# Performance work log

Hardware: AMD Instinct MI355X
Metric: run time of the kernel (lower is better)

## Reference

```python
import jax, jax.numpy as jnp
import numpy as np

SOS, EOS = 0, 1
MAXLEN = 128
EPS = 1e-5


def setup_inputs() -> dict:
    key = jax.random.key(0)
    ks = jax.random.split(key, 10)
    B, T, Hc, Hs, V, Hm = 64, 1024, 512, 512, 64, 128
    h = jax.random.normal(ks[0], (B, T, Hc), dtype=jnp.float32)
    x_seq_lens = jax.random.randint(ks[1], (B,), 1, T + 1).astype(jnp.int32)
    s = 0.05
    return {
        "h": h,
        "W_ih": jax.random.normal(ks[2], (4 * Hs, V + Hc), dtype=jnp.float32) * s,
        "W_hh": jax.random.normal(ks[3], (4 * Hs, Hs), dtype=jnp.float32) * s,
        "b_ih": jax.random.normal(ks[4], (4 * Hs,), dtype=jnp.float32) * s,
        "b_hh": jax.random.normal(ks[5], (4 * Hs,), dtype=jnp.float32) * s,
        "fc1_w": jax.random.normal(ks[6], (Hm, Hs + Hc), dtype=jnp.float32) * s,
        "fc1_b": jax.random.normal(ks[7], (Hm,), dtype=jnp.float32) * s,
        "fc2_w": jax.random.normal(ks[8], (V, Hm), dtype=jnp.float32) * s,
        "x_seq_lens": x_seq_lens,
    }


def reference(h, W_ih, W_hh, b_ih, b_hh, fc1_w, fc1_b, fc2_w, x_seq_lens):
    B, T, Hc = h.shape
    Hs = W_hh.shape[1]
    V = fc2_w.shape[0]
    # attention length mask [B, T]
    mask = (jnp.arange(T)[None, :] < x_seq_lens[:, None]).astype(h.dtype)
    sos = jax.nn.one_hot(jnp.full((B,), SOS), V, dtype=h.dtype)
    x0 = jnp.concatenate([sos, h[:, 0, :]], axis=-1)  # [B, V+Hc]
    carry0 = (x0, jnp.zeros((B, Hs), h.dtype), jnp.zeros((B, Hs), h.dtype),
              jnp.full((B,), MAXLEN, jnp.int32))

    def step(carry, t):
        x, hs, cs, lens = carry
        # single-layer LSTM cell, torch gate order i,f,g,o
        gates = x @ W_ih.T + hs @ W_hh.T + b_ih + b_hh
        i, f, g, o = jnp.split(gates, 4, axis=-1)
        cs = jax.nn.sigmoid(f) * cs + jax.nn.sigmoid(i) * jnp.tanh(g)
        hs = jax.nn.sigmoid(o) * jnp.tanh(cs)
        # dot-product attention (apply_proj=False, num_heads=1)
        e = jnp.einsum('bd,btd->bt', hs, h)
        exps = jnp.exp(e - jnp.max(e)) * mask  # MaskedSoftmax: global-max shift
        a = exps / (exps.sum(-1, keepdims=True) + EPS)
        ctx = jnp.einsum('bt,btd->bd', a, h)
        # chardist: two stacked linears (no nonlinearity), then softmax
        feat = jnp.concatenate([hs, ctx], axis=-1)
        logits = (feat @ fc1_w.T + fc1_b) @ fc2_w.T
        y_hat = jax.nn.softmax(logits, axis=-1)
        hit = (jnp.argmax(y_hat, axis=-1) == EOS) & (lens > t)
        lens = jnp.where(hit, t + 1, lens)
        x = jnp.concatenate([y_hat, ctx], axis=-1)  # decode mode (y=None)
        return (x, hs, cs, lens), (y_hat, a)

    (_, _, _, lens), (y_hats, atts) = jax.lax.scan(step, carry0, jnp.arange(MAXLEN))
    y_hats = jnp.transpose(y_hats, (1, 0, 2))              # [B, L, V]
    attentions = jnp.transpose(atts, (1, 0, 2))[:, None]   # [B, 1, L, T]
    return y_hats, lens, attentions
```

## Files before the change

kernel.cpp:

```cpp
#include <hip/hip_runtime.h>
#include <math.h>

typedef unsigned short ushort_t;
typedef unsigned int uint_t;

#define OFF_XT    0
#define OFF_CS    102400
#define OFF_E     135168
#define OFF_MD    200704
#define OFF_LENS  202752
#define OFF_W2    202816
#define OFF_B2    268352
#define OFF_CP    268416
#define OFF_HB16F 793600
#define WS_NEED   ((size_t)(793600 + 16777216) * 4)

#define OUT_YH   0
#define OUT_LENS 524288
#define OUT_ATT  524352

__device__ __forceinline__ float sigf(float x) { return 1.0f / (1.0f + __expf(-x)); }
__device__ __forceinline__ float dot4(float4 a, float4 b) {
    return a.x * b.x + a.y * b.y + a.z * b.z + a.w * b.w;
}
__device__ __forceinline__ uint_t bf16rne(float x) {
    uint_t u = __float_as_uint(x);
    return (u + 0x7FFFu + ((u >> 16) & 1u)) >> 16;
}
#define BLO(u) __uint_as_float((u) << 16)
#define BHI(u) __uint_as_float((u) & 0xFFFF0000u)

__global__ void k_init(const float* __restrict__ h, float* __restrict__ ws) {
    int blk = blockIdx.x, tid = threadIdx.x;
    int idx = blk * 256 + tid;
    if (idx < 102400) {
        int k = idx >> 6, b = idx & 63;
        float v = 0.0f;
        if (k == 0) v = 1.0f;
        else if (k >= 64 && k < 576) v = h[(size_t)b * 524288 + (k - 64)];
        ws[OFF_XT + idx] = v;
    }
    if (blk >= 400 && blk < 528)
        ws[OFF_CS + (blk - 400) * 256 + tid] = 0.0f;
    if (blk == 527 && tid < 64) ((int*)ws)[OFF_LENS + tid] = 128;
}

__global__ void k_hconv(const float* __restrict__ h, float* __restrict__ ws) {
    size_t i = ((size_t)blockIdx.x * 256 + threadIdx.x) * 8;
    float4 a = *(const float4*)(h + i);
    float4 b = *(const float4*)(h + i + 4);
    uint4 o;
    o.x = bf16rne(a.x) | (bf16rne(a.y) << 16);
    o.y = bf16rne(a.z) | (bf16rne(a.w) << 16);
    o.z = bf16rne(b.x) | (bf16rne(b.y) << 16);
    o.w = bf16rne(b.z) | (bf16rne(b.w) << 16);
    *(uint4*)((ushort_t*)(ws + OFF_HB16F) + i) = o;
}

__global__ void k_fuse(const float* __restrict__ fc1w, const float* __restrict__ fc1b,
                       const float* __restrict__ fc2w, float* __restrict__ ws) {
    int blk = blockIdx.x;
    int v = blk >> 2, kc = blk & 3;
    int k = kc * 256 + threadIdx.x;
    float acc = 0.0f;
#pragma unroll 8
    for (int m = 0; m < 128; m++) acc += fc2w[v * 128 + m] * fc1w[(size_t)m * 1024 + k];
    ws[OFF_W2 + (size_t)v * 1024 + k] = acc;
    if (kc == 0 && threadIdx.x == 0) {
        float bb = 0.0f;
        for (int m = 0; m < 128; m++) bb += fc2w[v * 128 + m] * fc1b[m];
        ws[OFF_B2 + v] = bb;
    }
}

__global__ void k_gates(const float* __restrict__ Wih, const float* __restrict__ Whh,
                        const float* __restrict__ bih, const float* __restrict__ bhh,
                        float* __restrict__ ws, int p) {
    const int tid = threadIdx.x;
    const int lane = tid & 63;
    const int w = tid >> 6;
    const int hs_in  = 576 + (p ? 512 : 0);
    const int hs_out = 576 + (p ? 0 : 512);
    __shared__ float gpart[4096];
    const int u0 = blockIdx.x * 2;
    const int wq = __builtin_amdgcn_readfirstlane(w);
    float acc[2][4] = {{0, 0, 0, 0}, {0, 0, 0, 0}};
    int k0 = wq * 136, k1 = k0 + 136;
    int kx1 = k1 < 576 ? k1 : 576;
#pragma unroll 2
    for (int k = k0; k < kx1; k += 4) {
        float4 xv;
        xv.x = ws[OFF_XT + (k + 0) * 64 + lane];
        xv.y = ws[OFF_XT + (k + 1) * 64 + lane];
        xv.z = ws[OFF_XT + (k + 2) * 64 + lane];
        xv.w = ws[OFF_XT + (k + 3) * 64 + lane];
#pragma unroll
        for (int uu = 0; uu < 2; ++uu)
#pragma unroll
            for (int g = 0; g < 4; ++g)
                acc[uu][g] += dot4(*(const float4*)&Wih[(size_t)(g * 512 + u0 + uu) * 576 + k], xv);
    }
    int kh0 = k0 > 576 ? k0 : 576;
#pragma unroll 2
    for (int k = kh0; k < k1; k += 4) {
        float4 xv;
        xv.x = ws[OFF_XT + (hs_in + (k - 576) + 0) * 64 + lane];
        xv.y = ws[OFF_XT + (hs_in + (k - 576) + 1) * 64 + lane];
        xv.z = ws[OFF_XT + (hs_in + (k - 576) + 2) * 64 + lane];
        xv.w = ws[OFF_XT + (hs_in + (k - 576) + 3) * 64 + lane];
#pragma unroll
        for (int uu = 0; uu < 2; ++uu)
#pragma unroll
            for (int g = 0; g < 4; ++g)
                acc[uu][g] += dot4(*(const float4*)&Whh[(size_t)(g * 512 + u0 + uu) * 512 + (k - 576)], xv);
    }
#pragma unroll
    for (int uu = 0; uu < 2; ++uu)
#pragma unroll
        for (int g = 0; g < 4; ++g)
            gpart[((w * 2 + uu) * 4 + g) * 64 + lane] = acc[uu][g];
    __syncthreads();
    if (tid < 128) {
        int uu = tid >> 6, b = tid & 63;
        int u = u0 + uu;
        float g4[4];
#pragma unroll
        for (int g = 0; g < 4; ++g) {
            float s = 0.0f;
#pragma unroll
            for (int ww = 0; ww < 8; ++ww) s += gpart[((ww * 2 + uu) * 4 + g) * 64 + b];
            g4[g] = s + bih[g * 512 + u] + bhh[g * 512 + u];
        }
        int idx = u * 64 + b;
        float co = ws[OFF_CS + idx];
        float I = sigf(g4[0]), F = sigf(g4[1]), G = tanhf(g4[2]), O = sigf(g4[3]);
        float cn = F * co + I * G;
        ws[OFF_CS + idx] = cn;
        ws[OFF_XT + (size_t)(hs_out + u) * 64 + b] = O * tanhf(cn);
    }
}

__global__ void k_attn16(const int* __restrict__ slen, float* __restrict__ ws, int p) {
    const int blk = blockIdx.x;
    const int tid = threadIdx.x;
    const int lane = tid & 63;
    const int w = tid >> 6;
    const int hs_out = 576 + (p ? 0 : 512);
    const int b = blk >> 4, sb = blk & 15;
    const int L = slen[b];
    const int t0 = sb * 64;
    __shared__ ushort_t stage[2][8192];
    __shared__ float hs_sh[512];
    __shared__ float e_sh[16];
    const ushort_t* hb = (const ushort_t*)(ws + OFF_HB16F) + ((size_t)b * 1024 + t0) * 512;
    uint4 r0 = *(const uint4*)(hb + tid * 8);
    uint4 r1 = *(const uint4*)(hb + 2048 + tid * 8);
    uint4 r2 = *(const uint4*)(hb + 4096 + tid * 8);
    uint4 r3 = *(const uint4*)(hb + 6144 + tid * 8);
    hs_sh[tid]       = ws[OFF_XT + (size_t)(hs_out + tid) * 64 + b];
    hs_sh[256 + tid] = ws[OFF_XT + (size_t)(hs_out + 256 + tid) * 64 + b];
    __syncthreads();
    float hsv[8];
#pragma unroll
    for (int j = 0; j < 8; ++j) hsv[j] = hs_sh[lane * 8 + j];
    float m_run = -INFINITY, D = 0.0f, accx = 0.0f, accy = 0.0f;
    int buf = 0;
    for (int c = 0; c < 4; ++c) {
        *(uint4*)&stage[buf][tid * 8]        = r0;
        *(uint4*)&stage[buf][tid * 8 + 2048] = r1;
        *(uint4*)&stage[buf][tid * 8 + 4096] = r2;
        *(uint4*)&stage[buf][tid * 8 + 6144] = r3;
        __syncthreads();
        if (c < 3) {
            const ushort_t* g = hb + (size_t)(c + 1) * 8192;
            r0 = *(const uint4*)(g + tid * 8);
            r1 = *(const uint4*)(g + 2048 + tid * 8);
            r2 = *(const uint4*)(g + 4096 + tid * 8);
            r3 = *(const uint4*)(g + 6144 + tid * 8);
        }
#pragma unroll
        for (int rr = 0; rr < 4; ++rr) {
            int tl = w * 4 + rr;
            uint4 hv = *(const uint4*)&stage[buf][tl * 512 + lane * 8];
            float part = BLO(hv.x) * hsv[0] + BHI(hv.x) * hsv[1]
                       + BLO(hv.y) * hsv[2] + BHI(hv.y) * hsv[3]
                       + BLO(hv.z) * hsv[4] + BHI(hv.z) * hsv[5]
                       + BLO(hv.w) * hsv[6] + BHI(hv.w) * hsv[7];
#pragma unroll
            for (int mm = 1; mm < 64; mm <<= 1) part += __shfl_xor(part, mm);
            if (lane == 0) {
                e_sh[tl] = part;
                ws[OFF_E + (size_t)b * 1024 + t0 + c * 16 + tl] = part;
            }
        }
        __syncthreads();
        float cm = e_sh[0];
#pragma unroll
        for (int j = 1; j < 16; ++j) cm = fmaxf(cm, e_sh[j]);
        float m_new = fmaxf(m_run, cm);
        float sc = __expf(m_run - m_new);
        accx *= sc; accy *= sc; D *= sc;
        m_run = m_new;
        const uint_t* st32 = (const uint_t*)&stage[buf][0];
#pragma unroll
        for (int tl = 0; tl < 16; ++tl) {
            int tg = t0 + c * 16 + tl;
            float wt = (tg < L) ? __expf(e_sh[tl] - m_run) : 0.0f;
            D += wt;
            uint_t v = st32[tl * 256 + tid];
            accx += wt * BLO(v);
            accy += wt * BHI(v);
        }
        buf ^= 1;
    }
    float2 o2; o2.x = accx; o2.y = accy;
    *(float2*)&ws[OFF_CP + (size_t)(b * 16 + sb) * 512 + tid * 2] = o2;
    if (tid == 0) {
        ws[OFF_MD + (b * 16 + sb) * 2]     = m_run;
        ws[OFF_MD + (b * 16 + sb) * 2 + 1] = D;
    }
}

__global__ void k_attn(const float* __restrict__ h, const int* __restrict__ slen,
                       float* __restrict__ ws, int p) {
    const int blk = blockIdx.x;
    const int tid = threadIdx.x;
    const int lane = tid & 63;
    const int w = tid >> 6;
    const int hs_out = 576 + (p ? 0 : 512);
    const int b = blk >> 4, sb = blk & 15;
    const int L = slen[b];
    const int t0 = sb * 64;
    __shared__ float stage[4096];
    __shared__ float hs_sh[512];
    __shared__ float e_sh[8];
    const float* hb = h + ((size_t)b * 1024 + t0) * 512;
    hs_sh[tid]       = ws[OFF_XT + (size_t)(hs_out + tid) * 64 + b];
    hs_sh[256 + tid] = ws[OFF_XT + (size_t)(hs_out + 256 + tid) * 64 + b];
    __syncthreads();
    float hsv[8];
#pragma unroll
    for (int j = 0; j < 8; ++j) hsv[j] = hs_sh[lane * 8 + j];
    float m_run = -INFINITY, D = 0.0f, accx = 0.0f, accy = 0.0f;
    for (int c = 0; c < 8; ++c) {
        const float* gsrc = hb + (size_t)c * 4096 + tid * 4;
        float4 tv0 = *(const float4*)(gsrc);
        float4 tv1 = *(const float4*)(gsrc + 1024);
        float4 tv2 = *(const float4*)(gsrc + 2048);
        float4 tv3 = *(const float4*)(gsrc + 3072);
        __syncthreads();
        *(float4*)&stage[tid * 4]        = tv0;
        *(float4*)&stage[1024 + tid * 4] = tv1;
        *(float4*)&stage[2048 + tid * 4] = tv2;
        *(float4*)&stage[3072 + tid * 4] = tv3;
        __syncthreads();
#pragma unroll
        for (int rr = 0; rr < 2; ++rr) {
            int tl = w * 2 + rr;
            const float4* rp = (const float4*)&stage[tl * 512 + lane * 8];
            float4 pp = rp[0], qq = rp[1];
            float part = pp.x * hsv[0] + pp.y * hsv[1] + pp.z * hsv[2] + pp.w * hsv[3]
                       + qq.x * hsv[4] + qq.y * hsv[5] + qq.z * hsv[6] + qq.w * hsv[7];
#pragma unroll
            for (int mm = 1; mm < 64; mm <<= 1) part += __shfl_xor(part, mm);
            if (lane == 0) {
                e_sh[tl] = part;
                ws[OFF_E + (size_t)b * 1024 + t0 + c * 8 + tl] = part;
            }
        }
        __syncthreads();
        float cm = e_sh[0];
#pragma unroll
        for (int j = 1; j < 8; ++j) cm = fmaxf(cm, e_sh[j]);
        float m_new = fmaxf(m_run, cm);
        float sc = __expf(m_run - m_new);
        accx *= sc; accy *= sc; D *= sc;
        m_run = m_new;
#pragma unroll
        for (int tl = 0; tl < 8; ++tl) {
            int tg = t0 + c * 8 + tl;
            float wt = (tg < L) ? __expf(e_sh[tl] - m_run) : 0.0f;
            D += wt;
            float2 hv = *(const float2*)&stage[tl * 512 + tid * 2];
            accx += wt * hv.x;
            accy += wt * hv.y;
        }
    }
    float2 o2; o2.x = accx; o2.y = accy;
    *(float2*)&ws[OFF_CP + (size_t)(b * 16 + sb) * 512 + tid * 2] = o2;
    if (tid == 0) {
        ws[OFF_MD + (b * 16 + sb) * 2]     = m_run;
        ws[OFF_MD + (b * 16 + sb) * 2 + 1] = D;
    }
}

__global__ void k_comb(const int* __restrict__ slen, float* __restrict__ ws,
                       float* __restrict__ out, int p, int ts) {
    const int b = blockIdx.x, tid = threadIdx.x;
    const int hs_out = 576 + (p ? 0 : 512);
    __shared__ float red[256];
    __shared__ float feat[1024];
    __shared__ float sc_sh[16];
    __shared__ float lg_s[64];
    float mx = -INFINITY;
#pragma unroll
    for (int i = 0; i < 4; ++i) mx = fmaxf(mx, ws[OFF_MD + (tid + 256 * i) * 2]);
    red[tid] = mx;
    __syncthreads();
    for (int s = 128; s > 0; s >>= 1) {
        if (tid < s) red[tid] = fmaxf(red[tid], red[tid + s]);
        __syncthreads();
    }
    float m_g = red[0];
    __syncthreads();
    if (tid < 16) {
        float mi = ws[OFF_MD + (b * 16 + tid) * 2];
        float Di = ws[OFF_MD + (b * 16 + tid) * 2 + 1];
        float s = __expf(mi - m_g);
        sc_sh[tid] = s;
        red[tid] = s * Di;
    }
    __syncthreads();
    float dn = 0.0f;
#pragma unroll
    for (int j = 0; j < 16; ++j) dn += red[j];
    float inv = 1.0f / (dn + 1e-5f);
    float cx = 0.0f, cy = 0.0f;
#pragma unroll 4
    for (int i = 0; i < 16; ++i) {
        float s = sc_sh[i];
        float2 v = *(const float2*)&ws[OFF_CP + (size_t)(b * 16 + i) * 512 + tid * 2];
        cx += s * v.x;
        cy += s * v.y;
    }
    cx *= inv; cy *= inv;
    feat[512 + tid * 2] = cx;
    feat[512 + tid * 2 + 1] = cy;
    ws[OFF_XT + (size_t)(64 + tid * 2) * 64 + b] = cx;
    ws[OFF_XT + (size_t)(64 + tid * 2 + 1) * 64 + b] = cy;
    feat[tid * 2]     = ws[OFF_XT + (size_t)(hs_out + tid * 2) * 64 + b];
    feat[tid * 2 + 1] = ws[OFF_XT + (size_t)(hs_out + tid * 2 + 1) * 64 + b];
    int L = slen[b];
#pragma unroll
    for (int q = 0; q < 4; ++q) {
        int t = tid + 256 * q;
        float e = ws[OFF_E + (size_t)b * 1024 + t];
        float a = (t < L) ? __expf(e - m_g) * inv : 0.0f;
        out[OUT_ATT + (size_t)b * 131072 + (size_t)ts * 1024 + t] = a;
    }
    __syncthreads();
    int v = tid >> 2, qq = tid & 3;
    const float4* w4 = (const float4*)(ws + OFF_W2 + (size_t)v * 1024 + qq * 256);
    const float4* f4 = (const float4*)feat + qq * 64;
    float acc = 0.0f;
#pragma unroll 8
    for (int k = 0; k < 64; ++k) acc += dot4(w4[k], f4[k]);
    acc += __shfl_xor(acc, 1);
    acc += __shfl_xor(acc, 2);
    if (qq == 0) lg_s[v] = acc;
    __syncthreads();
    if (tid < 64) {
        float lg = lg_s[tid] + ws[OFF_B2 + tid];
        float mxv = lg;
#pragma unroll
        for (int mm = 1; mm < 64; mm <<= 1) mxv = fmaxf(mxv, __shfl_xor(mxv, mm));
        float ev = __expf(lg - mxv);
        float s = ev;
#pragma unroll
        for (int mm = 1; mm < 64; mm <<= 1) s += __shfl_xor(s, mm);
        float y = ev / s;
        out[OUT_YH + (size_t)b * 8192 + ts * 64 + tid] = y;
        ws[OFF_XT + (size_t)tid * 64 + b] = y;
        float av = lg;
        int ai = tid;
#pragma unroll
        for (int mm = 1; mm < 64; mm <<= 1) {
            float ov = __shfl_xor(av, mm);
            int oi = __shfl_xor(ai, mm);
            if (ov > av || (ov == av && oi < ai)) { av = ov; ai = oi; }
        }
        if (tid == 0) {
            int* lens = (int*)ws + OFF_LENS;
            if (ai == 1 && lens[b] > ts) lens[b] = ts + 1;
        }
    }
}

__global__ void k_lens(const float* __restrict__ ws, float* __restrict__ out) {
    int tid = threadIdx.x;
    out[OUT_LENS + tid] = (float)(((const int*)ws)[OFF_LENS + tid]);
}

extern "C" void kernel_launch(void* const* d_in, const int* in_sizes, int n_in,
                              void* d_out, int out_size, void* d_ws, size_t ws_size,
                              hipStream_t stream) {
    (void)in_sizes; (void)n_in; (void)out_size;
    const float* h    = (const float*)d_in[0];
    const float* Wih  = (const float*)d_in[1];
    const float* Whh  = (const float*)d_in[2];
    const float* bih  = (const float*)d_in[3];
    const float* bhh  = (const float*)d_in[4];
    const float* fc1w = (const float*)d_in[5];
    const float* fc1b = (const float*)d_in[6];
    const float* fc2w = (const float*)d_in[7];
    const int*   slen = (const int*)d_in[8];
    float* ws  = (float*)d_ws;
    float* out = (float*)d_out;
    const bool use16 = (ws_size >= WS_NEED);

    k_init<<<528, 256, 0, stream>>>(h, ws);
    k_fuse<<<256, 256, 0, stream>>>(fc1w, fc1b, fc2w, ws);
    if (use16) k_hconv<<<16384, 256, 0, stream>>>(h, ws);
    for (int t = 0; t < 128; t++) {
        int p = t & 1;
        k_gates<<<256, 512, 0, stream>>>(Wih, Whh, bih, bhh, ws, p);
        if (use16) k_attn16<<<1024, 256, 0, stream>>>(slen, ws, p);
        else       k_attn<<<1024, 256, 0, stream>>>(h, slen, ws, p);
        k_comb<<<64, 256, 0, stream>>>(slen, ws, out, p, t);
    }
    k_lens<<<1, 64, 0, stream>>>(ws, out);
}
```

Before: 6.519 ms.

## Split bf16 attention into 32-row tiles, one-shot softmax, skip masked rows

The bf16 attention kernel now gives each block 32 time steps instead of 64 and launches twice as many blocks. Each block loads all its rows into registers at once, computes the scores while staging the data, and then does a single non-online softmax pass. The weighted sum stops at the valid length, so masked rows are skipped. The combine kernel takes the segment count as a parameter, and the lens copy is folded into the last combine step, removing one launch. The trade-off is more partial results to merge and higher register use per thread.

```diff
diff --git a/kernel.cpp b/kernel.cpp
--- a/kernel.cpp
+++ b/kernel.cpp
@@ -8,12 +8,12 @@
 #define OFF_CS    102400
 #define OFF_E     135168
 #define OFF_MD    200704
-#define OFF_LENS  202752
-#define OFF_W2    202816
-#define OFF_B2    268352
-#define OFF_CP    268416
-#define OFF_HB16F 793600
-#define WS_NEED   ((size_t)(793600 + 16777216) * 4)
+#define OFF_LENS  204800
+#define OFF_W2    204864
+#define OFF_B2    270400
+#define OFF_CP    270464
+#define OFF_HB16F 1319040
+#define WS_NEED   ((size_t)(1319040 + 16777216) * 4)
 
 #define OUT_YH   0
 #define OUT_LENS 524288
@@ -146,78 +146,72 @@
     const int lane = tid & 63;
     const int w = tid >> 6;
     const int hs_out = 576 + (p ? 0 : 512);
-    const int b = blk >> 4, sb = blk & 15;
+    const int b = blk >> 5, sb = blk & 31;
     const int L = slen[b];
-    const int t0 = sb * 64;
-    __shared__ ushort_t stage[2][8192];
+    const int t0 = sb * 32;
+    __shared__ ushort_t stage[16384];
     __shared__ float hs_sh[512];
-    __shared__ float e_sh[16];
+    __shared__ float e_sh[32];
+    __shared__ float wt_sh[32];
     const ushort_t* hb = (const ushort_t*)(ws + OFF_HB16F) + ((size_t)b * 1024 + t0) * 512;
-    uint4 r0 = *(const uint4*)(hb + tid * 8);
-    uint4 r1 = *(const uint4*)(hb + 2048 + tid * 8);
-    uint4 r2 = *(const uint4*)(hb + 4096 + tid * 8);
-    uint4 r3 = *(const uint4*)(hb + 6144 + tid * 8);
+    uint4 r0 = *(const uint4*)(hb + 0 * 2048 + tid * 8);
+    uint4 r1 = *(const uint4*)(hb + 1 * 2048 + tid * 8);
+    uint4 r2 = *(const uint4*)(hb + 2 * 2048 + tid * 8);
+    uint4 r3 = *(const uint4*)(hb + 3 * 2048 + tid * 8);
+    uint4 r4 = *(const uint4*)(hb + 4 * 2048 + tid * 8);
+    uint4 r5 = *(const uint4*)(hb + 5 * 2048 + tid * 8);
+    uint4 r6 = *(const uint4*)(hb + 6 * 2048 + tid * 8);
+    uint4 r7 = *(const uint4*)(hb + 7 * 2048 + tid * 8);
     hs_sh[tid]       = ws[OFF_XT + (size_t)(hs_out + tid) * 64 + b];
     hs_sh[256 + tid] = ws[OFF_XT + (size_t)(hs_out + 256 + tid) * 64 + b];
     __syncthreads();
     float hsv[8];
 #pragma unroll
     for (int j = 0; j < 8; ++j) hsv[j] = hs_sh[lane * 8 + j];
-    float m_run = -INFINITY, D = 0.0f, accx = 0.0f, accy = 0.0f;
-    int buf = 0;
-    for (int c = 0; c < 4; ++c) {
-        *(uint4*)&stage[buf][tid * 8]        = r0;
-        *(uint4*)&stage[buf][tid * 8 + 2048] = r1;
-        *(uint4*)&stage[buf][tid * 8 + 4096] = r2;
-        *(uint4*)&stage[buf][tid * 8 + 6144] = r3;
-        __syncthreads();
-        if (c < 3) {
-            const ushort_t* g = hb + (size_t)(c + 1) * 8192;
-            r0 = *(const uint4*)(g + tid * 8);
-            r1 = *(const uint4*)(g + 2048 + tid * 8);
-            r2 = *(const uint4*)(g + 4096 + tid * 8);
-            r3 = *(const uint4*)(g + 6144 + tid * 8);
-        }
-#pragma unroll
-        for (int rr = 0; rr < 4; ++rr) {
-            int tl = w * 4 + rr;
-            uint4 hv = *(const uint4*)&stage[buf][tl * 512 + lane * 8];
-            float part = BLO(hv.x) * hsv[0] + BHI(hv.x) * hsv[1]
-                       + BLO(hv.y) * hsv[2] + BHI(hv.y) * hsv[3]
-                       + BLO(hv.z) * hsv[4] + BHI(hv.z) * hsv[5]
-                       + BLO(hv.w) * hsv[6] + BHI(hv.w) * hsv[7];
-#pragma unroll
-            for (int mm = 1; mm < 64; mm <<= 1) part += __shfl_xor(part, mm);
-            if (lane == 0) {
-                e_sh[tl] = part;
-                ws[OFF_E + (size_t)b * 1024 + t0 + c * 16 + tl] = part;
-            }
-        }
-        __syncthreads();
-        float cm = e_sh[0];
-#pragma unroll
-        for (int j = 1; j < 16; ++j) cm = fmaxf(cm, e_sh[j]);
-        float m_new = fmaxf(m_run, cm);
-        float sc = __expf(m_run - m_new);
-        accx *= sc; accy *= sc; D *= sc;
-        m_run = m_new;
-        const uint_t* st32 = (const uint_t*)&stage[buf][0];
-#pragma unroll
-        for (int tl = 0; tl < 16; ++tl) {
-            int tg = t0 + c * 16 + tl;
-            float wt = (tg < L) ? __expf(e_sh[tl] - m_run) : 0.0f;
-            D += wt;
-            uint_t v = st32[tl * 256 + tid];
-            accx += wt * BLO(v);
-            accy += wt * BHI(v);
-        }
-        buf ^= 1;
+#define EROW(J, R)                                                                  \
+    {                                                                               \
+        float part = BLO(R.x) * hsv[0] + BHI(R.x) * hsv[1]                          \
+                   + BLO(R.y) * hsv[2] + BHI(R.y) * hsv[3]                          \
+                   + BLO(R.z) * hsv[4] + BHI(R.z) * hsv[5]                          \
+                   + BLO(R.w) * hsv[6] + BHI(R.w) * hsv[7];                         \
+        _Pragma("unroll")                                                           \
+        for (int mm = 1; mm < 64; mm <<= 1) part += __shfl_xor(part, mm);           \
+        if (lane == 0) e_sh[4 * (J) + w] = part;                                    \
+        *(uint4*)&stage[(J) * 2048 + tid * 8] = R;                                  \
+    }
+    EROW(0, r0) EROW(1, r1) EROW(2, r2) EROW(3, r3)
+    EROW(4, r4) EROW(5, r5) EROW(6, r6) EROW(7, r7)
+#undef EROW
+    __syncthreads();
+    float m_reg = 0.0f;
+    if (tid < 32) {
+        float m = e_sh[0];
+#pragma unroll
+        for (int j = 1; j < 32; ++j) m = fmaxf(m, e_sh[j]);
+        m_reg = m;
+        int tg = t0 + tid;
+        wt_sh[tid] = (tg < L) ? __expf(e_sh[tid] - m) : 0.0f;
+        ws[OFF_E + (size_t)b * 1024 + t0 + tid] = e_sh[tid];
+    }
+    __syncthreads();
+    int nr = L - t0;
+    nr = nr < 0 ? 0 : (nr > 32 ? 32 : nr);
+    float accx = 0.0f, accy = 0.0f;
+    const uint_t* st32 = (const uint_t*)stage;
+    for (int tl = 0; tl < nr; ++tl) {
+        float wt = wt_sh[tl];
+        uint_t v = st32[tl * 256 + tid];
+        accx += wt * BLO(v);
+        accy += wt * BHI(v);
     }
     float2 o2; o2.x = accx; o2.y = accy;
-    *(float2*)&ws[OFF_CP + (size_t)(b * 16 + sb) * 512 + tid * 2] = o2;
+    *(float2*)&ws[OFF_CP + (size_t)(b * 32 + sb) * 512 + tid * 2] = o2;
     if (tid == 0) {
-        ws[OFF_MD + (b * 16 + sb) * 2]     = m_run;
-        ws[OFF_MD + (b * 16 + sb) * 2 + 1] = D;
+        float D = 0.0f;
+#pragma unroll
+        for (int tl = 0; tl < 32; ++tl) D += wt_sh[tl];
+        ws[OFF_MD + (b * 32 + sb) * 2]     = m_reg;
+        ws[OFF_MD + (b * 32 + sb) * 2 + 1] = D;
     }
 }
 
@@ -295,16 +289,16 @@
 }
 
 __global__ void k_comb(const int* __restrict__ slen, float* __restrict__ ws,
-                       float* __restrict__ out, int p, int ts) {
+                       float* __restrict__ out, int p, int ts, int ns) {
     const int b = blockIdx.x, tid = threadIdx.x;
     const int hs_out = 576 + (p ? 0 : 512);
     __shared__ float red[256];
     __shared__ float feat[1024];
-    __shared__ float sc_sh[16];
+    __shared__ float sc_sh[32];
     __shared__ float lg_s[64];
+    const int nent = 64 * ns;
     float mx = -INFINITY;
-#pragma unroll
-    for (int i = 0; i < 4; ++i) mx = fmaxf(mx, ws[OFF_MD + (tid + 256 * i) * 2]);
+    for (int i = tid; i < nent; i += 256) mx = fmaxf(mx, ws[OFF_MD + i * 2]);
     red[tid] = mx;
     __syncthreads();
     for (int s = 128; s > 0; s >>= 1) {
@@ -313,23 +307,21 @@
     }
     float m_g = red[0];
     __syncthreads();
-    if (tid < 16) {
-        float mi = ws[OFF_MD + (b * 16 + tid) * 2];
-        float Di = ws[OFF_MD + (b * 16 + tid) * 2 + 1];
+    if (tid < ns) {
+        float mi = ws[OFF_MD + (b * ns + tid) * 2];
+        float Di = ws[OFF_MD + (b * ns + tid) * 2 + 1];
         float s = __expf(mi - m_g);
         sc_sh[tid] = s;
         red[tid] = s * Di;
     }
     __syncthreads();
     float dn = 0.0f;
-#pragma unroll
-    for (int j = 0; j < 16; ++j) dn += red[j];
+    for (int j = 0; j < ns; ++j) dn += red[j];
     float inv = 1.0f / (dn + 1e-5f);
     float cx = 0.0f, cy = 0.0f;
-#pragma unroll 4
-    for (int i = 0; i < 16; ++i) {
+    for (int i = 0; i < ns; ++i) {
         float s = sc_sh[i];
-        float2 v = *(const float2*)&ws[OFF_CP + (size_t)(b * 16 + i) * 512 + tid * 2];
+        float2 v = *(const float2*)&ws[OFF_CP + (size_t)(b * ns + i) * 512 + tid * 2];
         cx += s * v.x;
         cy += s * v.y;
     }
@@ -382,13 +374,9 @@
         if (tid == 0) {
             int* lens = (int*)ws + OFF_LENS;
             if (ai == 1 && lens[b] > ts) lens[b] = ts + 1;
+            if (ts == 127) out[OUT_LENS + b] = (float)lens[b];
         }
     }
-}
-
-__global__ void k_lens(const float* __restrict__ ws, float* __restrict__ out) {
-    int tid = threadIdx.x;
-    out[OUT_LENS + tid] = (float)(((const int*)ws)[OFF_LENS + tid]);
 }
 
 extern "C" void kernel_launch(void* const* d_in, const int* in_sizes, int n_in,
@@ -407,6 +395,7 @@
     float* ws  = (float*)d_ws;
     float* out = (float*)d_out;
     const bool use16 = (ws_size >= WS_NEED);
+    const int ns = use16 ? 32 : 16;
 
     k_init<<<528, 256, 0, stream>>>(h, ws);
     k_fuse<<<256, 256, 0, stream>>>(fc1w, fc1b, fc2w, ws);
@@ -414,9 +403,8 @@
     for (int t = 0; t < 128; t++) {
         int p = t & 1;
         k_gates<<<256, 512, 0, stream>>>(Wih, Whh, bih, bhh, ws, p);
-        if (use16) k_attn16<<<1024, 256, 0, stream>>>(slen, ws, p);
+        if (use16) k_attn16<<<2048, 256, 0, stream>>>(slen, ws, p);
         else       k_attn<<<1024, 256, 0, stream>>>(h, slen, ws, p);
-        k_comb<<<64, 256, 0, stream>>>(slen, ws, out, p, t);
-    }
-    k_lens<<<1, 64, 0, stream>>>(ws, out);
-}
+        k_comb<<<64, 256, 0, stream>>>(slen, ws, out, p, t, ns);
+    }
+}
```

Measured after the change: 6.536 ms. No clear change (+0.3%).
